# Kernel optimization log

Hardware: AMD Instinct MI355X
Metric: run time of the kernel (lower is better)

## Reference

```python
import jax, jax.numpy as jnp
import numpy as np

KERNEL_LEN = 128
INPUT_LEN = 1_000_000
MAX_PATH = 30          # hardcoded self.max_path in the module
PATH_NUM = 10          # self.path_num / out_len
L = INPUT_LEN + KERNEL_LEN  # max possible DTW path length


def setup_inputs() -> dict:
    key = jax.random.key(0)
    k1, k2, k3, k4, k5 = jax.random.split(key, 5)
    kernel = jax.random.normal(k1, (KERNEL_LEN,), dtype=jnp.float32)
    x = jax.random.normal(k2, (INPUT_LEN,), dtype=jnp.float32)
    # path indices produced by the external DP library (opaque int outputs)
    path_k = jax.random.randint(k3, (MAX_PATH, L), 0, KERNEL_LEN, dtype=jnp.int32)
    path_i = jax.random.randint(k4, (MAX_PATH, L), 0, INPUT_LEN, dtype=jnp.int32)
    path_length = jax.random.randint(k5, (MAX_PATH,), 0, L, dtype=jnp.int32)
    return {"kernel": kernel, "x": x, "path_k": path_k, "path_i": path_i,
            "path_length": path_length, "path_num": 12}


def reference(kernel, x, path_k, path_i, path_length, path_num):
    # out[k] = sum_{i < path_length[k]} (kernel[path_k[k,i]] - x[path_i[k,i]])**2
    # for k < min(path_num, PATH_NUM); remaining entries stay zero.
    n = min(int(path_num), PATH_NUM)
    pk = path_k[:PATH_NUM]                      # [PATH_NUM, L]
    pi = path_i[:PATH_NUM]
    step_mask = jnp.arange(L)[None, :] < path_length[:PATH_NUM, None]  # ragged lengths
    diff = kernel[pk] - x[pi]                   # gather + elementwise, [PATH_NUM, L]
    sq = jnp.where(step_mask, diff * diff, jnp.float32(0))
    out = sq.sum(axis=1)                        # [PATH_NUM]
    k_mask = jnp.arange(PATH_NUM) < n
    return jnp.where(k_mask, out, jnp.float32(0))
```

## Files before the change

kernel.cpp:

```cpp
#include <hip/hip_runtime.h>

#define KERNEL_LEN 128
#define INPUT_LEN 1000000
#define PATH_NUM 10
#define L_TOTAL (INPUT_LEN + KERNEL_LEN)
#define BLOCKS_PER_PATH 128
#define BLOCK_SIZE 256
#define CHUNK 16

typedef int v4i __attribute__((ext_vector_type(4)));

__global__ __launch_bounds__(BLOCK_SIZE) void dtw_spring_npath_kernel(
    const float* __restrict__ kern,
    const float* __restrict__ x,
    const int*   __restrict__ path_k,
    const int*   __restrict__ path_i,
    const int*   __restrict__ path_length,
    const int*   __restrict__ path_num,
    float*       __restrict__ out)
{
    __shared__ float k_lds[KERNEL_LEN];
    const int tid = threadIdx.x;
    if (tid < KERNEL_LEN) k_lds[tid] = kern[tid];
    __syncthreads();

    const int p = blockIdx.y;
    const int n = min(path_num[0], PATH_NUM);
    if (p >= n) return;

    const int len  = path_length[p];
    const int lenC = len & ~(CHUNK - 1);

    const int* __restrict__ pk = path_k + (size_t)p * L_TOTAL;
    const int* __restrict__ pi = path_i + (size_t)p * L_TOTAL;

    float acc = 0.0f;
    const int stride = gridDim.x * BLOCK_SIZE * CHUNK;
    for (int t0 = (blockIdx.x * BLOCK_SIZE + tid) * CHUNK; t0 < lenC; t0 += stride) {
        const v4i* pk4 = reinterpret_cast<const v4i*>(pk + t0);
        const v4i* pi4 = reinterpret_cast<const v4i*>(pi + t0);
        v4i ik[4], ii[4];
        #pragma unroll
        for (int c = 0; c < 4; ++c) ik[c] = __builtin_nontemporal_load(pk4 + c);
        #pragma unroll
        for (int c = 0; c < 4; ++c) ii[c] = __builtin_nontemporal_load(pi4 + c);

        float xs[CHUNK];
        #pragma unroll
        for (int c = 0; c < 4; ++c) {
            #pragma unroll
            for (int j = 0; j < 4; ++j)
                xs[c * 4 + j] = x[(unsigned)ii[c][j]];
        }
        #pragma unroll
        for (int c = 0; c < 4; ++c) {
            #pragma unroll
            for (int j = 0; j < 4; ++j) {
                const float d = k_lds[(unsigned)ik[c][j]] - xs[c * 4 + j];
                acc = fmaf(d, d, acc);
            }
        }
    }
    if (blockIdx.x == 0) {
        const int t = lenC + tid;
        if (t < len) {
            const float d = k_lds[pk[t]] - x[pi[t]];
            acc = fmaf(d, d, acc);
        }
    }

    #pragma unroll
    for (int off = 32; off > 0; off >>= 1)
        acc += __shfl_down(acc, off, 64);

    __shared__ float wsum[BLOCK_SIZE / 64];
    const int wave = tid >> 6;
    if ((tid & 63) == 0) wsum[wave] = acc;
    __syncthreads();
    if (tid == 0) {
        const float s = wsum[0] + wsum[1] + wsum[2] + wsum[3];
        atomicAdd(&out[p], s);
    }
}

extern "C" void kernel_launch(void* const* d_in, const int* in_sizes, int n_in,
                              void* d_out, int out_size, void* d_ws, size_t ws_size,
                              hipStream_t stream) {
    const float* kern        = (const float*)d_in[0];
    const float* x           = (const float*)d_in[1];
    const int*   path_k      = (const int*)d_in[2];
    const int*   path_i      = (const int*)d_in[3];
    const int*   path_length = (const int*)d_in[4];
    const int*   path_num    = (const int*)d_in[5];
    float*       out         = (float*)d_out;

    hipMemsetAsync(out, 0, (size_t)out_size * sizeof(float), stream);

    dim3 grid(BLOCKS_PER_PATH, PATH_NUM);
    dim3 block(BLOCK_SIZE);
    dtw_spring_npath_kernel<<<grid, block, 0, stream>>>(
        kern, x, path_k, path_i, path_length, path_num, out);
}
```

Baseline: 62.77 us.

## Bucket path records by x slice then gather from LDS-resident x tiles

Replaces the direct per-path gather with three kernels. A bucketing pass packs (path, x index, kernel index) into 32-bit records binned by 16K-element x slices. A gather pass loads each x slice into LDS and accumulates per-path squared differences. A final reduce adds partials and overflow records. This aims to turn random global x reads into LDS reads, at the cost of writing and re-reading an intermediate record buffer and adding two kernel launches.

```diff
diff --git a/kernel.cpp b/kernel.cpp
--- a/kernel.cpp
+++ b/kernel.cpp
@@ -4,82 +4,206 @@
 #define INPUT_LEN 1000000
 #define PATH_NUM 10
 #define L_TOTAL (INPUT_LEN + KERNEL_LEN)
-#define BLOCKS_PER_PATH 128
 #define BLOCK_SIZE 256
-#define CHUNK 16
+#define NWIN 977
+#define WAVES_A (NWIN * 4)
+#define NBUCKET 62
+#define BSHIFT 14
+#define SLICE (1 << BSHIFT)
+#define CAP 96
+#define NREGION (WAVES_A * NBUCKET)
+#define SPLIT 16
+#define NBLK_B (NBUCKET * SPLIT)
+#define OVF_CAP 4096
 
 typedef int v4i __attribute__((ext_vector_type(4)));
-
-__global__ __launch_bounds__(BLOCK_SIZE) void dtw_spring_npath_kernel(
-    const float* __restrict__ kern,
-    const float* __restrict__ x,
-    const int*   __restrict__ path_k,
-    const int*   __restrict__ path_i,
-    const int*   __restrict__ path_length,
-    const int*   __restrict__ path_num,
-    float*       __restrict__ out)
+typedef unsigned int u32;
+
+__global__ __launch_bounds__(BLOCK_SIZE) void dtw_bucket(
+    const int* __restrict__ path_k, const int* __restrict__ path_i,
+    const int* __restrict__ path_length, const int* __restrict__ path_num,
+    u32* __restrict__ counts, u32* __restrict__ recs,
+    u32* __restrict__ ovfcnt, u32* __restrict__ ovf)
 {
-    __shared__ float k_lds[KERNEL_LEN];
+    __shared__ u32 lcnt[4][NBUCKET];
+    __shared__ __align__(16) u32 stage[4][NBUCKET][32];
     const int tid = threadIdx.x;
-    if (tid < KERNEL_LEN) k_lds[tid] = kern[tid];
-    __syncthreads();
-
-    const int p = blockIdx.y;
-    const int n = min(path_num[0], PATH_NUM);
-    if (p >= n) return;
-
-    const int len  = path_length[p];
-    const int lenC = len & ~(CHUNK - 1);
-
-    const int* __restrict__ pk = path_k + (size_t)p * L_TOTAL;
-    const int* __restrict__ pi = path_i + (size_t)p * L_TOTAL;
-
-    float acc = 0.0f;
-    const int stride = gridDim.x * BLOCK_SIZE * CHUNK;
-    for (int t0 = (blockIdx.x * BLOCK_SIZE + tid) * CHUNK; t0 < lenC; t0 += stride) {
-        const v4i* pk4 = reinterpret_cast<const v4i*>(pk + t0);
-        const v4i* pi4 = reinterpret_cast<const v4i*>(pi + t0);
-        v4i ik[4], ii[4];
-        #pragma unroll
-        for (int c = 0; c < 4; ++c) ik[c] = __builtin_nontemporal_load(pk4 + c);
-        #pragma unroll
-        for (int c = 0; c < 4; ++c) ii[c] = __builtin_nontemporal_load(pi4 + c);
-
-        float xs[CHUNK];
-        #pragma unroll
-        for (int c = 0; c < 4; ++c) {
-            #pragma unroll
-            for (int j = 0; j < 4; ++j)
-                xs[c * 4 + j] = x[(unsigned)ii[c][j]];
-        }
-        #pragma unroll
-        for (int c = 0; c < 4; ++c) {
+    for (int i = tid; i < 4 * NBUCKET; i += BLOCK_SIZE) ((u32*)lcnt)[i] = 0u;
+    __syncthreads();
+
+    const int wave = tid >> 6;
+    const int lane = tid & 63;
+    const int wg   = blockIdx.x * 4 + wave;
+    const int n    = min(path_num[0], PATH_NUM);
+    const int w0   = blockIdx.x * 1024;
+
+    for (int p = 0; p < n; ++p) {
+        const int len = path_length[p];
+        if (w0 < len) {
+            const int t0 = w0 + tid * 4;
+            const int tl = min(t0, L_TOTAL - 4);
+            const v4i ik4 = *reinterpret_cast<const v4i*>(path_k + (size_t)p * L_TOTAL + tl);
+            const v4i ii4 = *reinterpret_cast<const v4i*>(path_i + (size_t)p * L_TOTAL + tl);
             #pragma unroll
             for (int j = 0; j < 4; ++j) {
-                const float d = k_lds[(unsigned)ik[c][j]] - xs[c * 4 + j];
-                acc = fmaf(d, d, acc);
+                if (t0 + j < len) {
+                    const u32 ii  = (u32)ii4[j];
+                    const u32 rec = ((u32)p << 27) | (ii << 7) | (u32)ik4[j];
+                    const u32 b   = ii >> BSHIFT;
+                    const u32 pos = atomicAdd(&lcnt[wave][b], 1u);
+                    if (pos < CAP) {
+                        stage[wave][b][pos & 31] = rec;
+                        if ((pos & 15) == 15) {
+                            const u32* s = &stage[wave][b][((pos >> 4) & 1) * 16];
+                            const u32 gb = ((u32)wg * NBUCKET + b) * CAP + (pos & ~15u);
+                            uint4 v0 = *(const uint4*)(s);
+                            uint4 v1 = *(const uint4*)(s + 4);
+                            uint4 v2 = *(const uint4*)(s + 8);
+                            uint4 v3 = *(const uint4*)(s + 12);
+                            *(uint4*)&recs[gb]      = v0;
+                            *(uint4*)&recs[gb + 4]  = v1;
+                            *(uint4*)&recs[gb + 8]  = v2;
+                            *(uint4*)&recs[gb + 12] = v3;
+                        }
+                    } else {
+                        const u32 op = atomicAdd(ovfcnt, 1u);
+                        if (op < OVF_CAP) ovf[op] = rec;
+                    }
+                }
             }
         }
     }
-    if (blockIdx.x == 0) {
-        const int t = lenC + tid;
-        if (t < len) {
-            const float d = k_lds[pk[t]] - x[pi[t]];
-            acc = fmaf(d, d, acc);
-        }
+    if (lane < NBUCKET) {
+        const u32 b  = (u32)lane;
+        const u32 c  = lcnt[wave][b];
+        const u32 cc = min(c, (u32)CAP);
+        counts[(u32)wg * NBUCKET + b] = cc;
+        const u32 base = ((u32)wg * NBUCKET + b) * CAP;
+        for (u32 k = c & ~15u; k < cc; ++k)
+            recs[base + k] = stage[wave][b][k & 31];
+    }
+}
+
+__global__ __launch_bounds__(BLOCK_SIZE) void dtw_gather(
+    const float* __restrict__ kern, const float* __restrict__ x,
+    const u32* __restrict__ counts, const u32* __restrict__ recs,
+    float* __restrict__ partials)
+{
+    __shared__ float xs[SLICE];
+    __shared__ float ks[KERNEL_LEN];
+    __shared__ float wsum[PATH_NUM][4];
+    const int tid = threadIdx.x;
+    const int b   = blockIdx.x;
+    const int s   = blockIdx.y;
+    if (tid < KERNEL_LEN) ks[tid] = kern[tid];
+    const int base = b << BSHIFT;
+    if (b < NBUCKET - 1) {
+        const float4* xsrc = (const float4*)(x + base);
+        float4* xdst = (float4*)xs;
+        for (int i = tid; i < SLICE / 4; i += BLOCK_SIZE) xdst[i] = xsrc[i];
+    } else {
+        for (int i = tid; i < SLICE; i += BLOCK_SIZE) {
+            const int g = base + i;
+            xs[i] = (g < INPUT_LEN) ? x[g] : 0.0f;
+        }
+    }
+    __syncthreads();
+
+    const int wave = tid >> 6;
+    const int lane = tid & 63;
+    float acc[PATH_NUM] = {};
+
+    int wg = s * 4 + wave;
+    u32 region = (u32)wg * NBUCKET + b;
+    u32 cnt_c = counts[region];
+    u32 rec_c = recs[region * CAP + lane];
+    while (wg < WAVES_A) {
+        const u32 cnt  = cnt_c;
+        const u32 rec0 = rec_c;
+        const u32 gb   = region * CAP;
+        const int wg2  = wg + 64;
+        if (wg2 < WAVES_A) {
+            const u32 r2 = (u32)wg2 * NBUCKET + b;
+            cnt_c = counts[r2];
+            rec_c = recs[r2 * CAP + lane];
+        }
+        if ((u32)lane < cnt) {
+            const u32 p  = rec0 >> 27;
+            const u32 ii = (rec0 >> 7) & 0xFFFFFu;
+            const float d = ks[rec0 & 127u] - xs[ii - base];
+            const float sq = d * d;
+            #pragma unroll
+            for (int P = 0; P < PATH_NUM; ++P)
+                acc[P] += (p == (u32)P) ? sq : 0.0f;
+        }
+        for (u32 st = 64; st < cnt; st += 64) {
+            if (st + lane < cnt) {
+                const u32 rec = recs[gb + st + lane];
+                const u32 p  = rec >> 27;
+                const u32 ii = (rec >> 7) & 0xFFFFFu;
+                const float d = ks[rec & 127u] - xs[ii - base];
+                const float sq = d * d;
+                #pragma unroll
+                for (int P = 0; P < PATH_NUM; ++P)
+                    acc[P] += (p == (u32)P) ? sq : 0.0f;
+            }
+        }
+        wg = wg2; region = (u32)wg * NBUCKET + b;
     }
 
     #pragma unroll
-    for (int off = 32; off > 0; off >>= 1)
-        acc += __shfl_down(acc, off, 64);
-
-    __shared__ float wsum[BLOCK_SIZE / 64];
-    const int wave = tid >> 6;
-    if ((tid & 63) == 0) wsum[wave] = acc;
-    __syncthreads();
-    if (tid == 0) {
-        const float s = wsum[0] + wsum[1] + wsum[2] + wsum[3];
-        atomicAdd(&out[p], s);
+    for (int P = 0; P < PATH_NUM; ++P) {
+        float v = acc[P];
+        #pragma unroll
+        for (int off = 32; off > 0; off >>= 1) v += __shfl_down(v, off, 64);
+        if (lane == 0) wsum[P][wave] = v;
+    }
+    __syncthreads();
+    if (tid < PATH_NUM) {
+        const int blkid = s * NBUCKET + b;
+        partials[(size_t)blkid * PATH_NUM + tid] =
+            wsum[tid][0] + wsum[tid][1] + wsum[tid][2] + wsum[tid][3];
+    }
+}
+
+__global__ __launch_bounds__(BLOCK_SIZE) void dtw_reduce(
+    const float* __restrict__ kern, const float* __restrict__ x,
+    const float* __restrict__ partials, const u32* __restrict__ ovfcnt,
+    const u32* __restrict__ ovf, const int* __restrict__ path_num,
+    float* __restrict__ out)
+{
+    const int tid = threadIdx.x;
+    float acc[PATH_NUM] = {};
+    for (int t = tid; t < NBLK_B; t += BLOCK_SIZE) {
+        #pragma unroll
+        for (int P = 0; P < PATH_NUM; ++P)
+            acc[P] += partials[(size_t)t * PATH_NUM + P];
+    }
+    const u32 oc = min(*ovfcnt, (u32)OVF_CAP);
+    for (u32 i = tid; i < oc; i += BLOCK_SIZE) {
+        const u32 rec = ovf[i];
+        const u32 p  = rec >> 27;
+        const u32 ii = (rec >> 7) & 0xFFFFFu;
+        const float d = kern[rec & 127u] - x[ii];
+        const float sq = d * d;
+        #pragma unroll
+        for (int P = 0; P < PATH_NUM; ++P)
+            acc[P] += (p == (u32)P) ? sq : 0.0f;
+    }
+    __shared__ float wsum[PATH_NUM][4];
+    const int wave = tid >> 6, lane = tid & 63;
+    #pragma unroll
+    for (int P = 0; P < PATH_NUM; ++P) {
+        float v = acc[P];
+        #pragma unroll
+        for (int off = 32; off > 0; off >>= 1) v += __shfl_down(v, off, 64);
+        if (lane == 0) wsum[P][wave] = v;
+    }
+    __syncthreads();
+    const int n = min(path_num[0], PATH_NUM);
+    if (tid < PATH_NUM) {
+        const float sv = wsum[tid][0] + wsum[tid][1] + wsum[tid][2] + wsum[tid][3];
+        out[tid] = (tid < n) ? sv : 0.0f;
     }
 }
 
@@ -94,10 +218,18 @@
     const int*   path_num    = (const int*)d_in[5];
     float*       out         = (float*)d_out;
 
-    hipMemsetAsync(out, 0, (size_t)out_size * sizeof(float), stream);
-
-    dim3 grid(BLOCKS_PER_PATH, PATH_NUM);
-    dim3 block(BLOCK_SIZE);
-    dtw_spring_npath_kernel<<<grid, block, 0, stream>>>(
-        kern, x, path_k, path_i, path_length, path_num, out);
-}
+    u32* counts   = (u32*)d_ws;
+    u32* ovfcnt   = counts + NREGION;
+    u32* ovf      = counts + NREGION + 8;
+    u32* recs     = counts + NREGION + 8 + OVF_CAP;
+    float* partials = (float*)(recs + (size_t)NREGION * CAP);
+
+    hipMemsetAsync(counts, 0, (size_t)(NREGION + 1) * sizeof(u32), stream);
+
+    dtw_bucket<<<dim3(NWIN), dim3(BLOCK_SIZE), 0, stream>>>(
+        path_k, path_i, path_length, path_num, counts, recs, ovfcnt, ovf);
+    dtw_gather<<<dim3(NBUCKET, SPLIT), dim3(BLOCK_SIZE), 0, stream>>>(
+        kern, x, counts, recs, partials);
+    dtw_reduce<<<dim3(1), dim3(BLOCK_SIZE), 0, stream>>>(
+        kern, x, partials, ovfcnt, ovf, path_num, out);
+}
```

Result: slower. 94.16 us (+50.0%).
